# Kernel optimization log

Hardware: AMD Instinct MI355X
Metric: run time of the kernel (lower is better)

Reference implementation:

```python
import jax, jax.numpy as jnp
import numpy as np

R_MIN, R_MAX, MAX_PHASE = 0.9, 0.999, 6.283
BN_EPS = 1e-5


def _lru(x, nu_log, theta_log, B_re, B_im, C_re, C_im, D):
    # x: [B,T,E]; diagonal LRU with complex state of size H
    lam = jnp.exp(-jnp.exp(nu_log) + 1j * jnp.exp(theta_log))          # [H] complex
    gamma = jnp.sqrt(jnp.maximum(1.0 - jnp.abs(lam) ** 2, 1e-12))      # [H]
    Bc = B_re + 1j * B_im                                               # [H,E]
    Cc = C_re + 1j * C_im                                               # [E,H]
    Bu = jnp.einsum('bte,he->bth', x.astype(jnp.complex64), Bc) * gamma  # [B,T,H]

    def step(h, u):
        h = lam * h + u
        return h, h

    h0 = jnp.zeros((x.shape[0], lam.shape[0]), jnp.complex64)
    _, hs = jax.lax.scan(step, h0, jnp.swapaxes(Bu, 0, 1))              # [T,B,H]
    hs = jnp.swapaxes(hs, 0, 1)                                         # [B,T,H]
    return jnp.einsum('bth,eh->bte', hs, Cc).real + D * x               # [B,T,E]


def _batchnorm(x, scale, bias):
    # normalize over (batch, time), feature axis last
    mu = jnp.mean(x, axis=(0, 1))
    var = jnp.var(x, axis=(0, 1))
    return (x - mu) * jax.lax.rsqrt(var + BN_EPS) * scale + bias


def _glu(x):
    a, b = jnp.split(x, 2, axis=-1)
    return a * jax.nn.sigmoid(b)


def setup_inputs() -> dict:
    key = jax.random.key(0)
    ks = jax.random.split(key, 16)
    B, T, TS, E, H, L, O, NB = 32, 2048, 64, 256, 256, 1024, 10, 6
    u1 = jax.random.uniform(ks[0], (NB, H))
    u2 = jax.random.uniform(ks[1], (NB, H))
    nu_log = jnp.log(-0.5 * jnp.log(u1 * (R_MAX**2 - R_MIN**2) + R_MIN**2))
    theta_log = jnp.log(MAX_PHASE * u2)
    return {
        'x': jax.random.normal(ks[2], (B, T, TS), jnp.float32),
        'W_enc': jax.random.normal(ks[3], (TS, E), jnp.float32) / np.sqrt(TS),
        'b_enc': jnp.zeros((E,), jnp.float32),
        'nu_log': nu_log.astype(jnp.float32),
        'theta_log': theta_log.astype(jnp.float32),
        'B_re': jax.random.normal(ks[4], (NB, H, E), jnp.float32) / np.sqrt(2 * E),
        'B_im': jax.random.normal(ks[5], (NB, H, E), jnp.float32) / np.sqrt(2 * E),
        'C_re': jax.random.normal(ks[6], (NB, E, H), jnp.float32) / np.sqrt(H),
        'C_im': jax.random.normal(ks[7], (NB, E, H), jnp.float32) / np.sqrt(H),
        'D': jax.random.normal(ks[8], (NB, E), jnp.float32),
        'W1': jax.random.normal(ks[9], (NB, E, L), jnp.float32) / np.sqrt(E),
        'b1': jnp.zeros((NB, L), jnp.float32),
        'W2': jax.random.normal(ks[10], (NB, L // 2, E), jnp.float32) / np.sqrt(L // 2),
        'b2': jnp.zeros((NB, E), jnp.float32),
        'bn_scale': jnp.ones((NB, E), jnp.float32),
        'bn_bias': jnp.zeros((NB, E), jnp.float32),
        'W_out': jax.random.normal(ks[11], (E, O), jnp.float32) / np.sqrt(E),
        'b_out': jnp.zeros((O,), jnp.float32),
    }


def reference(x, W_enc, b_enc, nu_log, theta_log, B_re, B_im, C_re, C_im, D,
              W1, b1, W2, b2, bn_scale, bn_bias, W_out, b_out):
    x = x @ W_enc + b_enc                      # [B,T,E]
    y = x                                       # residual anchor (same for every block)
    for i in range(6):
        h = _batchnorm(x, bn_scale[i], bn_bias[i])
        h = _lru(h, nu_log[i], theta_log[i], B_re[i], B_im[i], C_re[i], C_im[i], D[i])
        h = _glu(h @ W1[i] + b1[i])             # dropout is identity (p=0 / eval)
        h = h @ W2[i] + b2[i]
        x = h + y
    pooled = jnp.mean(x, axis=1)                # pool=True head: mean over time
    return pooled @ W_out + b_out               # [B, out_dim]
```

## Files before the change

### kernel.cpp

```cpp
#include <hip/hip_runtime.h>
#include <hip/hip_bf16.h>
#include <math.h>

using bf16 = __hip_bfloat16;
typedef __attribute__((ext_vector_type(8))) short s8v;
typedef __attribute__((ext_vector_type(4))) float f4v;

#define MTOT 65536
#define TLEN 2048
#define NCHUNK 32
#define TCH 64

__device__ __forceinline__ float b2f(bf16 x) { return __bfloat162float(x); }
__device__ __forceinline__ bf16 f2b(float x) { return __float2bfloat16(x); }
__device__ __forceinline__ float bits2f(unsigned short u) {
    unsigned int x = ((unsigned int)u) << 16; float f; __builtin_memcpy(&f, &x, 4); return f;
}
__device__ __forceinline__ unsigned short f2bits(float x) {
    bf16 h = f2b(x); unsigned short u; __builtin_memcpy(&u, &h, 2); return u;
}

__device__ __forceinline__ float ldf(const void* p, size_t i, int f) {
    return f ? ((const float*)p)[i] : b2f(((const bf16*)p)[i]);
}

__device__ __forceinline__ void ld_g2l(const void* g, void* l) {
    __builtin_amdgcn_global_load_lds(
        (const __attribute__((address_space(1))) void*)g,
        (__attribute__((address_space(3))) void*)l,
        16, 0, 0);
}

__global__ void detect_k(const unsigned short* __restrict__ x, int* __restrict__ flag) {
    int tid = threadIdx.x;
    int cnt = 0;
    for (int i = tid; i < 8192; i += 256) {
        int e = (x[i] >> 7) & 0xFF;
        if (e == 0 || e == 0xFF) cnt++;
    }
    __shared__ int red[256];
    red[tid] = cnt;
    __syncthreads();
    for (int s = 128; s > 0; s >>= 1) {
        if (tid < s) red[tid] += red[tid + s];
        __syncthreads();
    }
    if (tid == 0) flag[0] = (red[0] >= 2) ? 1 : 0;
}

__global__ void cvt_k(const void* __restrict__ src, bf16* __restrict__ dst, int n,
                      const int* __restrict__ flag) {
    int f = *flag;
    int i = blockIdx.x * 256 + threadIdx.x;
    if (i < n) dst[i] = f2b(ldf(src, i, f));
}

__global__ void cvt_small(const void* b_enc, const void* Dp, const void* b1, const void* b2,
                          const void* bn_s, const void* bn_b, const void* W_out, const void* b_out,
                          bf16* b_encb, bf16* Db, bf16* b1b, bf16* b2b, bf16* bnsb, bf16* bnbb,
                          bf16* Woutb, bf16* boutb, const int* __restrict__ flag) {
    int f = *flag;
    int blk = blockIdx.x, t = threadIdx.x;
    const void* src; bf16* dst; int base, n;
    if (blk < 1)       { src = b_enc; dst = b_encb; base = blk;      n = 256; }
    else if (blk < 7)  { src = Dp;    dst = Db;     base = blk - 1;  n = 1536; }
    else if (blk < 31) { src = b1;    dst = b1b;    base = blk - 7;  n = 6144; }
    else if (blk < 37) { src = b2;    dst = b2b;    base = blk - 31; n = 1536; }
    else if (blk < 43) { src = bn_s;  dst = bnsb;   base = blk - 37; n = 1536; }
    else if (blk < 49) { src = bn_b;  dst = bnbb;   base = blk - 43; n = 1536; }
    else if (blk < 59) { src = W_out; dst = Woutb;  base = blk - 49; n = 2560; }
    else               { src = b_out; dst = boutb;  base = 0;        n = 10; }
    int i = base * 256 + t;
    if (i < n) dst[i] = f2b(ldf(src, i, f));
}

__global__ void lamgam_k(const void* __restrict__ nu, const void* __restrict__ th,
                         float* __restrict__ lamb, float* __restrict__ gamt,
                         const int* __restrict__ flag) {
    int f = *flag;
    int g = blockIdx.x * 256 + threadIdx.x;
    float nl = ldf(nu, g, f), tl = ldf(th, g, f);
    float mag = expf(-expf(nl));
    float ang = expf(tl);
    lamb[g * 2] = mag * cosf(ang);
    lamb[g * 2 + 1] = mag * sinf(ang);
    gamt[g] = sqrtf(fmaxf(1.f - mag * mag, 1e-12f));
}

template<int KK, int NBN, int EPI>
__global__ __launch_bounds__(256)
void gemm_v6(const bf16* __restrict__ A, const bf16* __restrict__ W,
             bf16* __restrict__ outB, bf16* __restrict__ outB2, int ldo,
             const bf16* __restrict__ bias,
             const bf16* __restrict__ Dv, const bf16* __restrict__ aux,
             const float* __restrict__ fstats, float* __restrict__ spart)
{
    constexpr int LG = (NBN == 8) ? 3 : 2;
    const int id = blockIdx.x;
    const int xcd = id & 7, q = id >> 3;
    const int bn = q & (NBN - 1);
    const int bm = (q >> LG) * 8 + xcd;

    const int tid = threadIdx.x;
    const int lane = tid & 63, wv = tid >> 6;
    const int wm = wv >> 1, wn = wv & 1;
    const int quad = lane >> 4, cl = lane & 15;

    __shared__ __align__(16) short As[2][128 * 32];
    __shared__ __align__(16) short Ws[2][64 * 32];
    __shared__ float sred[256];

    const char* Ab = (const char*)A + (size_t)bm * 128 * ((size_t)KK * 2);
    const char* Wb = (const char*)W + (size_t)bn * 64 * ((size_t)KK * 2);
    constexpr int ldb = KK * 2;

    auto stage = [&](int t, int bi) {
        const int kb = t * 64;
#pragma unroll
        for (int it = 0; it < 2; ++it) {
            int G = it * 256 + tid;
            int r = G >> 2;
            int gl = (G & 3) ^ ((r >> 1) & 3);
            ld_g2l(Ab + (size_t)r * ldb + kb + gl * 16,
                   (char*)As[bi] + (it * 4 + wv) * 1024);
        }
        {
            int r = tid >> 2;
            int gl = (tid & 3) ^ ((r >> 1) & 3);
            ld_g2l(Wb + (size_t)r * ldb + kb + gl * 16,
                   (char*)Ws[bi] + wv * 1024);
        }
    };

    f4v acc[4][2];
#pragma unroll
    for (int i = 0; i < 4; i++)
#pragma unroll
        for (int j = 0; j < 2; j++) acc[i][j] = (f4v){0.f, 0.f, 0.f, 0.f};

    constexpr int NT = KK >> 5;
    stage(0, 0);
#pragma unroll 2
    for (int t = 0; t < NT; ++t) {
        const int cur = t & 1;
        if (t + 1 < NT) {
            stage(t + 1, cur ^ 1);
            asm volatile("s_waitcnt vmcnt(3)" ::: "memory");
        } else {
            asm volatile("s_waitcnt vmcnt(0)" ::: "memory");
        }
        asm volatile("s_barrier" ::: "memory");
        const char* Ac = (const char*)As[cur];
        const char* Wc = (const char*)Ws[cur];
        s8v af[4], bw[2];
#pragma unroll
        for (int i = 0; i < 4; i++) {
            int r = wm * 64 + i * 16 + cl;
            af[i] = *(const s8v*)(Ac + r * 64 + ((quad ^ ((r >> 1) & 3)) * 16));
        }
#pragma unroll
        for (int j = 0; j < 2; j++) {
            int r = wn * 32 + j * 16 + cl;
            bw[j] = *(const s8v*)(Wc + r * 64 + ((quad ^ ((r >> 1) & 3)) * 16));
        }
#pragma unroll
        for (int i = 0; i < 4; i++)
#pragma unroll
            for (int j = 0; j < 2; j++)
                acc[i][j] = __builtin_amdgcn_mfma_f32_16x16x32_bf16(af[i], bw[j], acc[i][j], 0, 0, 0);
        asm volatile("s_barrier" ::: "memory");
    }

    const size_t ld = (size_t)ldo;
    constexpr bool STATS = (EPI == 1 || EPI == 5);
#pragma unroll
    for (int j = 0; j < 2; j++) {
        float ss = 0.f, ss2 = 0.f;
        const int n = bn * 64 + wn * 32 + j * 16 + cl;
#pragma unroll
        for (int i = 0; i < 4; i++) {
#pragma unroll
            for (int r4 = 0; r4 < 4; r4++) {
                int m = bm * 128 + wm * 64 + i * 16 + quad * 4 + r4;
                size_t idx = (size_t)m * ld + n;
                float v = acc[i][j][r4];
                if (EPI == 1) {
                    v += b2f(bias[n]);
                    outB[idx] = f2b(v);
                    outB2[idx] = f2b(v);
                } else if (EPI == 2) {
                    v += b2f(Dv[n]) * (fstats[n] * b2f(aux[idx]) + fstats[256 + n]);
                    outB[idx] = f2b(v);
                } else if (EPI == 5) {
                    v += b2f(bias[n]) + b2f(aux[idx]);
                    outB[idx] = f2b(v);
                } else if (EPI == 6) {
                    v += fstats[n];
                    outB[idx] = f2b(v);
                }
                if (STATS) { ss += v; ss2 += v * v; }
            }
        }
        if (STATS) {
            ss += __shfl_xor(ss, 16);  ss += __shfl_xor(ss, 32);
            ss2 += __shfl_xor(ss2, 16); ss2 += __shfl_xor(ss2, 32);
            if (lane < 16) {
                int nl = wn * 32 + j * 16 + lane;
                sred[wm * 64 + nl] = ss;
                sred[128 + wm * 64 + nl] = ss2;
            }
        }
    }
    if constexpr (STATS) {
        __syncthreads();
        if (tid < 64) {
            float sv = sred[tid] + sred[64 + tid];
            float sv2 = sred[128 + tid] + sred[192 + tid];
            spart[(size_t)bm * 256 + bn * 64 + tid] = sv;
            spart[131072 + (size_t)bm * 256 + bn * 64 + tid] = sv2;
        }
    }
}

__global__ __launch_bounds__(256)
void glu_v6(const bf16* __restrict__ A, const bf16* __restrict__ W,
            bf16* __restrict__ outB, const bf16* __restrict__ bias)
{
    constexpr int KK = 256;
    const int id = blockIdx.x;
    const int xcd = id & 7, q = id >> 3;
    const int nb = q & 7;
    const int bm = (q >> 3) * 8 + xcd;

    const int tid = threadIdx.x;
    const int lane = tid & 63, wv = tid >> 6;
    const int wm = wv >> 1, wn = wv & 1;
    const int quad = lane >> 4, cl = lane & 15;

    __shared__ __align__(16) short As[2][128 * 32];
    __shared__ __align__(16) short Vs[2][64 * 32];
    __shared__ __align__(16) short Gs[2][64 * 32];

    const char* Ab = (const char*)A + (size_t)bm * 128 * ((size_t)KK * 2);
    const char* Vb = (const char*)W + (size_t)(nb * 64) * ((size_t)KK * 2);
    const char* Gb = (const char*)W + (size_t)(512 + nb * 64) * ((size_t)KK * 2);
    constexpr int ldb = KK * 2;

    auto stage = [&](int t, int bi) {
        const int kb = t * 64;
#pragma unroll
        for (int it = 0; it < 2; ++it) {
            int G = it * 256 + tid;
            int r = G >> 2;
            int gl = (G & 3) ^ ((r >> 1) & 3);
            ld_g2l(Ab + (size_t)r * ldb + kb + gl * 16,
                   (char*)As[bi] + (it * 4 + wv) * 1024);
        }
        {
            int r = tid >> 2;
            int gl = (tid & 3) ^ ((r >> 1) & 3);
            ld_g2l(Vb + (size_t)r * ldb + kb + gl * 16, (char*)Vs[bi] + wv * 1024);
            ld_g2l(Gb + (size_t)r * ldb + kb + gl * 16, (char*)Gs[bi] + wv * 1024);
        }
    };

    f4v accv[4][2], accg[4][2];
#pragma unroll
    for (int i = 0; i < 4; i++)
#pragma unroll
        for (int j = 0; j < 2; j++) {
            accv[i][j] = (f4v){0.f, 0.f, 0.f, 0.f};
            accg[i][j] = (f4v){0.f, 0.f, 0.f, 0.f};
        }

    constexpr int NT = KK >> 5;
    stage(0, 0);
#pragma unroll 2
    for (int t = 0; t < NT; ++t) {
        const int cur = t & 1;
        if (t + 1 < NT) {
            stage(t + 1, cur ^ 1);
            asm volatile("s_waitcnt vmcnt(4)" ::: "memory");
        } else {
            asm volatile("s_waitcnt vmcnt(0)" ::: "memory");
        }
        asm volatile("s_barrier" ::: "memory");
        const char* Ac = (const char*)As[cur];
        const char* Vc = (const char*)Vs[cur];
        const char* Gc = (const char*)Gs[cur];
        s8v af[4], bv[2], bg[2];
#pragma unroll
        for (int i = 0; i < 4; i++) {
            int r = wm * 64 + i * 16 + cl;
            af[i] = *(const s8v*)(Ac + r * 64 + ((quad ^ ((r >> 1) & 3)) * 16));
        }
#pragma unroll
        for (int j = 0; j < 2; j++) {
            int r = wn * 32 + j * 16 + cl;
            int off = r * 64 + ((quad ^ ((r >> 1) & 3)) * 16);
            bv[j] = *(const s8v*)(Vc + off);
            bg[j] = *(const s8v*)(Gc + off);
        }
#pragma unroll
        for (int i = 0; i < 4; i++)
#pragma unroll
            for (int j = 0; j < 2; j++) {
                accv[i][j] = __builtin_amdgcn_mfma_f32_16x16x32_bf16(af[i], bv[j], accv[i][j], 0, 0, 0);
                accg[i][j] = __builtin_amdgcn_mfma_f32_16x16x32_bf16(af[i], bg[j], accg[i][j], 0, 0, 0);
            }
        asm volatile("s_barrier" ::: "memory");
    }

#pragma unroll
    for (int i = 0; i < 4; i++) {
#pragma unroll
        for (int j = 0; j < 2; j++) {
#pragma unroll
            for (int r4 = 0; r4 < 4; r4++) {
                int m = bm * 128 + wm * 64 + i * 16 + quad * 4 + r4;
                int n = nb * 64 + wn * 32 + j * 16 + cl;
                float v = accv[i][j][r4] + b2f(bias[n]);
                float g = accg[i][j][r4] + b2f(bias[512 + n]);
                outB[(size_t)m * 512 + n] = f2b(v * (1.f / (1.f + __expf(-g))));
            }
        }
    }
}

__global__ void bn_finish2(const float* __restrict__ part, float* __restrict__ stats,
                           const bf16* __restrict__ sc, const bf16* __restrict__ bi) {
    int e = blockIdx.x;
    int t = threadIdx.x;
    float s = part[(size_t)t * 256 + e] + part[(size_t)(t + 256) * 256 + e];
    float s2 = part[131072 + (size_t)t * 256 + e] + part[131072 + (size_t)(t + 256) * 256 + e];
    __shared__ float rs[256], rs2[256];
    rs[t] = s; rs2[t] = s2;
    __syncthreads();
    for (int k = 128; k > 0; k >>= 1) {
        if (t < k) { rs[t] += rs[t + k]; rs2[t] += rs2[t + k]; }
        __syncthreads();
    }
    if (t == 0) {
        float mu = rs[0] * (1.f / 65536.f);
        float var = rs2[0] * (1.f / 65536.f) - mu * mu;
        float a = rsqrtf(var + 1e-5f) * b2f(sc[e]);
        stats[e] = a;
        stats[256 + e] = b2f(bi[e]) - mu * a;
    }
}

__global__ void pack_wb(const void* __restrict__ B_re, const void* __restrict__ B_im,
                        size_t off, const float* __restrict__ gam,
                        const float* __restrict__ stats,
                        bf16* __restrict__ out, float* __restrict__ bias_out,
                        const int* __restrict__ flag) {
    int f = *flag;
    int n = blockIdx.x;
    int e = threadIdx.x;
    int h = n >> 1;
    const void* src = (n & 1) ? B_im : B_re;
    float v = ldf(src, off + (size_t)h * 256 + e, f);
    out[(size_t)n * 256 + e] = f2b(v * gam[h] * stats[e]);
    __shared__ float rs[256];
    rs[e] = v * stats[256 + e];
    __syncthreads();
    for (int k = 128; k > 0; k >>= 1) {
        if (e < k) rs[e] += rs[e + k];
        __syncthreads();
    }
    if (e == 0) bias_out[n] = rs[0] * gam[h];
}

__global__ void pack_l(const void* __restrict__ C_re, const void* __restrict__ C_im,
                       const void* __restrict__ W1, const void* __restrict__ W2,
                       size_t offC, size_t offW1, size_t offW2,
                       bf16* __restrict__ wc, bf16* __restrict__ w1t, bf16* __restrict__ w2t,
                       const int* __restrict__ flag) {
    int f = *flag;
    int blk = blockIdx.x;
    if (blk < 512) {
        int g = blk * 256 + threadIdx.x;
        int e = g >> 9, k = g & 511, h = k >> 1;
        float v = ldf((k & 1) ? C_im : C_re, offC + (size_t)e * 256 + h, f);
        wc[g] = f2b((k & 1) ? -v : v);
    } else if (blk < 1536) {
        int g = (blk - 512) * 256 + threadIdx.x;
        int n = g >> 8, k = g & 255;
        w1t[g] = f2b(ldf(W1, offW1 + (size_t)k * 1024 + n, f));
    } else {
        int g = (blk - 1536) * 256 + threadIdx.x;
        int n = g >> 9, k = g & 511;
        w2t[g] = f2b(ldf(W2, offW2 + (size_t)k * 256 + n, f));
    }
}

__global__ void lru_carry(const bf16* __restrict__ bu, const float* __restrict__ lam,
                          float* __restrict__ carry) {
    int gg = blockIdx.x * 256 + threadIdx.x;
    int hp = gg & 127, c = (gg >> 7) & 31, b = gg >> 12;
    f4v lm = *(const f4v*)&lam[hp * 4];
    float sr0 = 0.f, si0 = 0.f, sr1 = 0.f, si1 = 0.f;
    const char* p = (const char*)(bu + ((size_t)(b * TLEN + c * TCH)) * 512) + hp * 8;
    for (int t = 0; t < TCH; t++) {
        unsigned long long u = *(const unsigned long long*)p;
        float ur0 = bits2f((unsigned short)u), ui0 = bits2f((unsigned short)(u >> 16));
        float ur1 = bits2f((unsigned short)(u >> 32)), ui1 = bits2f((unsigned short)(u >> 48));
        float nr0 = lm[0] * sr0 - lm[1] * si0 + ur0;
        si0 = lm[0] * si0 + lm[1] * sr0 + ui0; sr0 = nr0;
        float nr1 = lm[2] * sr1 - lm[3] * si1 + ur1;
        si1 = lm[2] * si1 + lm[3] * sr1 + ui1; sr1 = nr1;
        p += 1024;
    }
    *(f4v*)&carry[(size_t)gg * 4] = (f4v){sr0, si0, sr1, si1};
}

__global__ void lru_prefix(const float* __restrict__ carry, float* __restrict__ pre,
                           const float* __restrict__ lam) {
    int g = blockIdx.x * 256 + threadIdx.x;
    int h = g & 255, b = g >> 8;
    float pr = lam[h * 2], pi = lam[h * 2 + 1];
    for (int k = 0; k < 6; k++) { float nr = pr * pr - pi * pi; pi = 2.f * pr * pi; pr = nr; }
    float er = 0.f, ei = 0.f;
    for (int c = 0; c < NCHUNK; c++) {
        size_t idx = ((size_t)(b * NCHUNK + c) * 256 + h) * 2;
        pre[idx] = er; pre[idx + 1] = ei;
        float cr = carry[idx], ci = carry[idx + 1];
        float nr = pr * er - pi * ei + cr;
        ei = pr * ei + pi * er + ci;
        er = nr;
    }
}

__global__ void lru_final(bf16* __restrict__ bu, const float* __restrict__ pre,
                          const float* __restrict__ lam) {
    int gg = blockIdx.x * 256 + threadIdx.x;
    int hp = gg & 127, c = (gg >> 7) & 31, b = gg >> 12;
    f4v lm = *(const f4v*)&lam[hp * 4];
    f4v st = *(const f4v*)&pre[(size_t)gg * 4];
    float sr0 = st[0], si0 = st[1], sr1 = st[2], si1 = st[3];
    char* p = (char*)(bu + ((size_t)(b * TLEN + c * TCH)) * 512) + hp * 8;
    for (int t = 0; t < TCH; t++) {
        unsigned long long u = *(const unsigned long long*)p;
        float ur0 = bits2f((unsigned short)u), ui0 = bits2f((unsigned short)(u >> 16));
        float ur1 = bits2f((unsigned short)(u >> 32)), ui1 = bits2f((unsigned short)(u >> 48));
        float nr0 = lm[0] * sr0 - lm[1] * si0 + ur0;
        si0 = lm[0] * si0 + lm[1] * sr0 + ui0; sr0 = nr0;
        float nr1 = lm[2] * sr1 - lm[3] * si1 + ur1;
        si1 = lm[2] * si1 + lm[3] * sr1 + ui1; sr1 = nr1;
        unsigned long long w = (unsigned long long)f2bits(sr0)
                             | ((unsigned long long)f2bits(si0) << 16)
                             | ((unsigned long long)f2bits(sr1) << 32)
                             | ((unsigned long long)f2bits(si1) << 48);
        *(unsigned long long*)p = w;
        p += 1024;
    }
}

__global__ void head_k(const float* __restrict__ part, const bf16* __restrict__ W_out,
                       const bf16* __restrict__ b_out, void* __restrict__ out,
                       const int* __restrict__ flag) {
    int b = blockIdx.x;
    int tid = threadIdx.x;
    __shared__ float sp[256];
    __shared__ float red[160];
    float s = 0.f;
    for (int c = 0; c < 16; c++) s += part[((size_t)(b * 16 + c)) * 256 + tid];
    sp[tid] = s * (1.f / 2048.f);
    __syncthreads();
    if (tid < 160) {
        int o = tid >> 4, sg = tid & 15;
        float a = 0.f;
        for (int e = sg; e < 256; e += 16) a += sp[e] * b2f(W_out[e * 10 + o]);
        red[tid] = a;
    }
    __syncthreads();
    if (tid < 10) {
        float acc = b2f(b_out[tid]);
        for (int sg = 0; sg < 16; sg++) acc += red[tid * 16 + sg];
        if (*flag) ((float*)out)[b * 10 + tid] = acc;
        else       ((bf16*)out)[b * 10 + tid] = f2b(acc);
    }
}

__global__ void pack_wt_enc(const void* __restrict__ W_enc, bf16* __restrict__ out,
                            const int* __restrict__ flag) {
    int f = *flag;
    int g = blockIdx.x * 256 + threadIdx.x;
    int n = g >> 6, k = g & 63;
    out[g] = f2b(ldf(W_enc, (size_t)k * 256 + n, f));
}

extern "C" void kernel_launch(void* const* d_in, const int* in_sizes, int n_in,
                              void* d_out, int out_size, void* d_ws, size_t ws_size,
                              hipStream_t stream) {
    (void)in_sizes; (void)n_in; (void)out_size; (void)ws_size;
    const void* x      = d_in[0];
    const void* W_enc  = d_in[1];
    const void* b_enc  = d_in[2];
    const void* nu_log = d_in[3];
    const void* th_log = d_in[4];
    const void* B_re   = d_in[5];
    const void* B_im   = d_in[6];
    const void* C_re   = d_in[7];
    const void* C_im   = d_in[8];
    const void* Dp     = d_in[9];
    const void* W1     = d_in[10];
    const void* b1     = d_in[11];
    const void* W2     = d_in[12];
    const void* b2     = d_in[13];
    const void* bn_s   = d_in[14];
    const void* bn_b   = d_in[15];
    const void* W_out  = d_in[16];
    const void* b_out  = d_in[17];

    char* w = (char*)d_ws;
    bf16* xc  = (bf16*)w; w += (size_t)MTOT * 256 * 2;
    bf16* y   = (bf16*)w; w += (size_t)MTOT * 256 * 2;
    bf16* hbn = (bf16*)w; w += (size_t)MTOT * 256 * 2;
    bf16* bu  = (bf16*)w; w += (size_t)MTOT * 512 * 2;
    float* stats  = (float*)w; w += 4096;
    float* bnpart = (float*)w; w += 1048576;
    float* carry  = (float*)w; w += 2097152;
    float* pre    = (float*)w; w += 2097152;
    float* lamb   = (float*)w; w += 12288;
    float* gamt   = (float*)w; w += 6144;
    float* bubias = (float*)w; w += 2048;
    int*   flag   = (int*)w;  w += 256;
    bf16* wt_enc = (bf16*)w; w += 32768;
    bf16* wb  = (bf16*)w; w += 262144;
    bf16* wc  = (bf16*)w; w += 262144;
    bf16* w1t = (bf16*)w; w += 524288;
    bf16* w2t = (bf16*)w; w += 262144;
    bf16* b_encb = (bf16*)w; w += 512;
    bf16* Db     = (bf16*)w; w += 3072;
    bf16* b1b    = (bf16*)w; w += 12288;
    bf16* b2b    = (bf16*)w; w += 3072;
    bf16* bnsb   = (bf16*)w; w += 3072;
    bf16* bnbb   = (bf16*)w; w += 3072;
    bf16* Woutb  = (bf16*)w; w += 5120;
    bf16* boutb  = (bf16*)w; w += 32;
    bf16* xb = bu;

    dim3 blk(256);
    detect_k<<<1, blk, 0, stream>>>((const unsigned short*)x, flag);
    cvt_k<<<16384, blk, 0, stream>>>(x, xb, 4194304, flag);
    cvt_small<<<60, blk, 0, stream>>>(b_enc, Dp, b1, b2, bn_s, bn_b, W_out, b_out,
                                      b_encb, Db, b1b, b2b, bnsb, bnbb, Woutb, boutb, flag);
    lamgam_k<<<6, blk, 0, stream>>>(nu_log, th_log, lamb, gamt, flag);
    pack_wt_enc<<<64, blk, 0, stream>>>(W_enc, wt_enc, flag);

    gemm_v6<64, 4, 1><<<2048, blk, 0, stream>>>(xb, wt_enc, xc, y, 256,
                                                b_encb, nullptr, nullptr, nullptr, bnpart);
    for (int i = 0; i < 6; ++i) {
        bn_finish2<<<256, blk, 0, stream>>>(bnpart, stats, bnsb + i * 256, bnbb + i * 256);
        pack_wb<<<512, blk, 0, stream>>>(B_re, B_im, (size_t)i * 65536, gamt + i * 256,
                                         stats, wb, bubias, flag);
        gemm_v6<256, 8, 6><<<4096, blk, 0, stream>>>(xc, wb, bu, nullptr, 512,
                                                     nullptr, nullptr, nullptr, bubias, nullptr);
        lru_carry<<<512, blk, 0, stream>>>(bu, lamb + i * 512, carry);
        lru_prefix<<<32, blk, 0, stream>>>(carry, pre, lamb + i * 512);
        lru_final<<<512, blk, 0, stream>>>(bu, pre, lamb + i * 512);
        pack_l<<<2048, blk, 0, stream>>>(C_re, C_im, W1, W2,
                                         (size_t)i * 65536, (size_t)i * 262144, (size_t)i * 131072,
                                         wc, w1t, w2t, flag);
        gemm_v6<512, 4, 2><<<2048, blk, 0, stream>>>(bu, wc, hbn, nullptr, 256,
                                                     nullptr, Db + i * 256, xc, stats, nullptr);
        glu_v6<<<4096, blk, 0, stream>>>(hbn, w1t, bu, b1b + i * 1024);
        gemm_v6<512, 4, 5><<<2048, blk, 0, stream>>>(bu, w2t, xc, nullptr, 256,
                                                     b2b + i * 256, nullptr, y, nullptr, bnpart);
    }
    head_k<<<32, blk, 0, stream>>>(bnpart, Woutb, boutb, d_out, flag);
}
```

Before: 1.449 ms.

## Triple-buffer GEMM LDS pipeline and batch weight packing for all layers upfront

The GEMM and GLU kernels move from double to triple LDS buffering: they prefetch two K-tiles ahead and wait with deeper vmcnt counts, so global loads get more time to overlap with MFMA work. The per-layer pack_l launch is replaced by one pack_all launch before the loop that packs C, W1 and W2 for all six layers into larger workspace buffers. This removes six kernel launches from the layer loop. In exchange, LDS use per block rises, which may lower occupancy, and the weight workspace grows sixfold.

```diff
diff --git a/kernel.cpp b/kernel.cpp
--- a/kernel.cpp
+++ b/kernel.cpp
@@ -89,7 +89,7 @@
 
 template<int KK, int NBN, int EPI>
 __global__ __launch_bounds__(256)
-void gemm_v6(const bf16* __restrict__ A, const bf16* __restrict__ W,
+void gemm_v7(const bf16* __restrict__ A, const bf16* __restrict__ W,
              bf16* __restrict__ outB, bf16* __restrict__ outB2, int ldo,
              const bf16* __restrict__ bias,
              const bf16* __restrict__ Dv, const bf16* __restrict__ aux,
@@ -106,8 +106,8 @@
     const int wm = wv >> 1, wn = wv & 1;
     const int quad = lane >> 4, cl = lane & 15;
 
-    __shared__ __align__(16) short As[2][128 * 32];
-    __shared__ __align__(16) short Ws[2][64 * 32];
+    __shared__ __align__(16) short As[3][128 * 32];
+    __shared__ __align__(16) short Ws[3][64 * 32];
     __shared__ float sred[256];
 
     const char* Ab = (const char*)A + (size_t)bm * 128 * ((size_t)KK * 2);
@@ -140,18 +140,20 @@
 
     constexpr int NT = KK >> 5;
     stage(0, 0);
-#pragma unroll 2
+    if (NT > 1) stage(1, 1);
+#pragma unroll
     for (int t = 0; t < NT; ++t) {
-        const int cur = t & 1;
-        if (t + 1 < NT) {
-            stage(t + 1, cur ^ 1);
+        if (t + 2 < NT) {
+            stage(t + 2, (t + 2) % 3);
+            asm volatile("s_waitcnt vmcnt(6)" ::: "memory");
+        } else if (t + 1 < NT) {
             asm volatile("s_waitcnt vmcnt(3)" ::: "memory");
         } else {
             asm volatile("s_waitcnt vmcnt(0)" ::: "memory");
         }
         asm volatile("s_barrier" ::: "memory");
-        const char* Ac = (const char*)As[cur];
-        const char* Wc = (const char*)Ws[cur];
+        const char* Ac = (const char*)As[t % 3];
+        const char* Wc = (const char*)Ws[t % 3];
         s8v af[4], bw[2];
 #pragma unroll
         for (int i = 0; i < 4; i++) {
@@ -223,7 +225,7 @@
 }
 
 __global__ __launch_bounds__(256)
-void glu_v6(const bf16* __restrict__ A, const bf16* __restrict__ W,
+void glu_v7(const bf16* __restrict__ A, const bf16* __restrict__ W,
             bf16* __restrict__ outB, const bf16* __restrict__ bias)
 {
     constexpr int KK = 256;
@@ -237,9 +239,9 @@
     const int wm = wv >> 1, wn = wv & 1;
     const int quad = lane >> 4, cl = lane & 15;
 
-    __shared__ __align__(16) short As[2][128 * 32];
-    __shared__ __align__(16) short Vs[2][64 * 32];
-    __shared__ __align__(16) short Gs[2][64 * 32];
+    __shared__ __align__(16) short As[3][128 * 32];
+    __shared__ __align__(16) short Vs[3][64 * 32];
+    __shared__ __align__(16) short Gs[3][64 * 32];
 
     const char* Ab = (const char*)A + (size_t)bm * 128 * ((size_t)KK * 2);
     const char* Vb = (const char*)W + (size_t)(nb * 64) * ((size_t)KK * 2);
@@ -275,19 +277,21 @@
 
     constexpr int NT = KK >> 5;
     stage(0, 0);
-#pragma unroll 2
+    stage(1, 1);
+#pragma unroll
     for (int t = 0; t < NT; ++t) {
-        const int cur = t & 1;
-        if (t + 1 < NT) {
-            stage(t + 1, cur ^ 1);
+        if (t + 2 < NT) {
+            stage(t + 2, (t + 2) % 3);
+            asm volatile("s_waitcnt vmcnt(8)" ::: "memory");
+        } else if (t + 1 < NT) {
             asm volatile("s_waitcnt vmcnt(4)" ::: "memory");
         } else {
             asm volatile("s_waitcnt vmcnt(0)" ::: "memory");
         }
         asm volatile("s_barrier" ::: "memory");
-        const char* Ac = (const char*)As[cur];
-        const char* Vc = (const char*)Vs[cur];
-        const char* Gc = (const char*)Gs[cur];
+        const char* Ac = (const char*)As[t % 3];
+        const char* Vc = (const char*)Vs[t % 3];
+        const char* Gc = (const char*)Gs[t % 3];
         s8v af[4], bv[2], bg[2];
 #pragma unroll
         for (int i = 0; i < 4; i++) {
@@ -371,26 +375,27 @@
     if (e == 0) bias_out[n] = rs[0] * gam[h];
 }
 
-__global__ void pack_l(const void* __restrict__ C_re, const void* __restrict__ C_im,
-                       const void* __restrict__ W1, const void* __restrict__ W2,
-                       size_t offC, size_t offW1, size_t offW2,
-                       bf16* __restrict__ wc, bf16* __restrict__ w1t, bf16* __restrict__ w2t,
-                       const int* __restrict__ flag) {
+__global__ void pack_all(const void* __restrict__ C_re, const void* __restrict__ C_im,
+                         const void* __restrict__ W1, const void* __restrict__ W2,
+                         bf16* __restrict__ wc6, bf16* __restrict__ w1t6, bf16* __restrict__ w2t6,
+                         const int* __restrict__ flag) {
     int f = *flag;
-    int blk = blockIdx.x;
+    int L = blockIdx.x >> 11;
+    int blk = blockIdx.x & 2047;
+    size_t offC = (size_t)L * 65536, offW1 = (size_t)L * 262144, offW2 = (size_t)L * 131072;
     if (blk < 512) {
         int g = blk * 256 + threadIdx.x;
         int e = g >> 9, k = g & 511, h = k >> 1;
         float v = ldf((k & 1) ? C_im : C_re, offC + (size_t)e * 256 + h, f);
-        wc[g] = f2b((k & 1) ? -v : v);
+        wc6[(size_t)L * 131072 + g] = f2b((k & 1) ? -v : v);
     } else if (blk < 1536) {
         int g = (blk - 512) * 256 + threadIdx.x;
         int n = g >> 8, k = g & 255;
-        w1t[g] = f2b(ldf(W1, offW1 + (size_t)k * 1024 + n, f));
+        w1t6[(size_t)L * 262144 + g] = f2b(ldf(W1, offW1 + (size_t)k * 1024 + n, f));
     } else {
         int g = (blk - 1536) * 256 + threadIdx.x;
         int n = g >> 9, k = g & 511;
-        w2t[g] = f2b(ldf(W2, offW2 + (size_t)k * 256 + n, f));
+        w2t6[(size_t)L * 131072 + g] = f2b(ldf(W2, offW2 + (size_t)k * 256 + n, f));
     }
 }
 
@@ -527,10 +532,10 @@
     float* bubias = (float*)w; w += 2048;
     int*   flag   = (int*)w;  w += 256;
     bf16* wt_enc = (bf16*)w; w += 32768;
-    bf16* wb  = (bf16*)w; w += 262144;
-    bf16* wc  = (bf16*)w; w += 262144;
-    bf16* w1t = (bf16*)w; w += 524288;
-    bf16* w2t = (bf16*)w; w += 262144;
+    bf16* wb   = (bf16*)w; w += 262144;
+    bf16* wc6  = (bf16*)w; w += 6 * 262144;
+    bf16* w1t6 = (bf16*)w; w += 6 * 524288;
+    bf16* w2t6 = (bf16*)w; w += 6 * 262144;
     bf16* b_encb = (bf16*)w; w += 512;
     bf16* Db     = (bf16*)w; w += 3072;
     bf16* b1b    = (bf16*)w; w += 12288;
@@ -548,25 +553,23 @@
                                       b_encb, Db, b1b, b2b, bnsb, bnbb, Woutb, boutb, flag);
     lamgam_k<<<6, blk, 0, stream>>>(nu_log, th_log, lamb, gamt, flag);
     pack_wt_enc<<<64, blk, 0, stream>>>(W_enc, wt_enc, flag);
-
-    gemm_v6<64, 4, 1><<<2048, blk, 0, stream>>>(xb, wt_enc, xc, y, 256,
+    pack_all<<<12288, blk, 0, stream>>>(C_re, C_im, W1, W2, wc6, w1t6, w2t6, flag);
+
+    gemm_v7<64, 4, 1><<<2048, blk, 0, stream>>>(xb, wt_enc, xc, y, 256,
                                                 b_encb, nullptr, nullptr, nullptr, bnpart);
     for (int i = 0; i < 6; ++i) {
         bn_finish2<<<256, blk, 0, stream>>>(bnpart, stats, bnsb + i * 256, bnbb + i * 256);
         pack_wb<<<512, blk, 0, stream>>>(B_re, B_im, (size_t)i * 65536, gamt + i * 256,
                                          stats, wb, bubias, flag);
-        gemm_v6<256, 8, 6><<<4096, blk, 0, stream>>>(xc, wb, bu, nullptr, 512,
+        gemm_v7<256, 8, 6><<<4096, blk, 0, stream>>>(xc, wb, bu, nullptr, 512,
                                                      nullptr, nullptr, nullptr, bubias, nullptr);
         lru_carry<<<512, blk, 0, stream>>>(bu, lamb + i * 512, carry);
         lru_prefix<<<32, blk, 0, stream>>>(carry, pre, lamb + i * 512);
         lru_final<<<512, blk, 0, stream>>>(bu, pre, lamb + i * 512);
-        pack_l<<<2048, blk, 0, stream>>>(C_re, C_im, W1, W2,
-                                         (size_t)i * 65536, (size_t)i * 262144, (size_t)i * 131072,
-                                         wc, w1t, w2t, flag);
-        gemm_v6<512, 4, 2><<<2048, blk, 0, stream>>>(bu, wc, hbn, nullptr, 256,
+        gemm_v7<512, 4, 2><<<2048, blk, 0, stream>>>(bu, wc6 + (size_t)i * 131072, hbn, nullptr, 256,
                                                      nullptr, Db + i * 256, xc, stats, nullptr);
-        glu_v6<<<4096, blk, 0, stream>>>(hbn, w1t, bu, b1b + i * 1024);
-        gemm_v6<512, 4, 5><<<2048, blk, 0, stream>>>(bu, w2t, xc, nullptr, 256,
+        glu_v7<<<4096, blk, 0, stream>>>(hbn, w1t6 + (size_t)i * 262144, bu, b1b + i * 1024);
+        gemm_v7<512, 4, 5><<<2048, blk, 0, stream>>>(bu, w2t6 + (size_t)i * 131072, xc, nullptr, 256,
                                                      b2b + i * 256, nullptr, y, nullptr, bnpart);
     }
     head_k<<<32, blk, 0, stream>>>(bnpart, Woutb, boutb, d_out, flag);
```

Result: faster. 1.393 ms (-3.9%).
